# Kernel tuning notes

Hardware: AMD Instinct MI355X
Metric: run time of the kernel (lower is better)

The kernel has to match this reference:

```python
import jax, jax.numpy as jnp
import numpy as np

B, D_IN, H = 8192, 4096, 128
E, N, C = 3, 256, 32          # experts, codebook_size, codebook_dim
D1, D2 = 512, 256             # down_units
U1, U2 = 256, 512             # up_units
CW = 0.25                     # commitment_weight


def setup_inputs() -> dict:
    key = jax.random.key(0)
    ks = jax.random.split(key, 16)
    s = 0.02
    f32 = jnp.float32
    inp = {
        'x':   jax.random.normal(ks[0], (B, D_IN), f32),
        # llm_down MLP: 4096 -> 512 -> 256 -> 128 (ReLU on hiddens, linear out)
        'Wd1': jax.random.normal(ks[1], (D_IN, D1), f32) * s, 'bd1': jnp.zeros((D1,), f32),
        'Wd2': jax.random.normal(ks[2], (D1, D2), f32) * s,  'bd2': jnp.zeros((D2,), f32),
        'Wd3': jax.random.normal(ks[3], (D2, H), f32) * s,   'bd3': jnp.zeros((H,), f32),
        # per-expert VQ: project_in 128->32, codebook [256,32], project_out 32->128
        'Win':  jax.random.normal(ks[4], (E, H, C), f32) * s, 'bin_': jnp.zeros((E, C), f32),
        'codebook': jax.random.normal(ks[5], (E, N, C), f32),
        'Wout': jax.random.normal(ks[6], (E, C, H), f32) * s, 'bout': jnp.zeros((E, H), f32),
        # llm_up MLP: 128 -> 256 -> 512 -> 4096
        'Wu1': jax.random.normal(ks[7], (H, U1), f32) * s,   'bu1': jnp.zeros((U1,), f32),
        'Wu2': jax.random.normal(ks[8], (U1, U2), f32) * s,  'bu2': jnp.zeros((U2,), f32),
        'Wu3': jax.random.normal(ks[9], (U2, D_IN), f32) * s, 'bu3': jnp.zeros((D_IN,), f32),
    }
    return inp


def _decorrelation_loss(qemb):
    # qemb: [B, E, H]
    b, e, h = qemb.shape
    cen = qemb - qemb.mean(axis=0, keepdims=True)
    cen = cen.transpose(1, 0, 2).reshape(e, -1)          # [E, B*H]
    cov = (cen @ cen.T) / (b * h - 1)                    # [E, E]
    std = jnp.sqrt(jnp.diag(cov))
    std = jnp.where(std > 1e-8, std, 1.0)
    corr = cov / jnp.outer(std, std)
    c2 = corr ** 2
    return c2.sum() - jnp.diag(c2).sum()


def _vq_experts(latent, Win, bin_, codebook, Wout, bout):
    # latent: [B,H]; all experts share the same (unmasked) latent.
    xe = jnp.einsum('bh,ehc->ebc', latent, Win) + bin_[:, None, :]      # [E,B,C]
    d2 = ((xe ** 2).sum(-1)[..., None]
          - 2.0 * jnp.einsum('ebc,enc->ebn', xe, codebook)
          + (codebook ** 2).sum(-1)[:, None, :])                        # [E,B,N]
    idx = jnp.argmin(d2, axis=-1)                                       # [E,B]
    q = jax.vmap(lambda c, i: c[i])(codebook, idx)                      # [E,B,C] gather
    commit = CW * jnp.mean((jax.lax.stop_gradient(q) - xe) ** 2, axis=(1, 2)).sum()
    quant = xe + jax.lax.stop_gradient(q - xe)                          # straight-through
    qe = jnp.einsum('ebc,ech->ebh', quant, Wout) + bout[:, None, :]     # [E,B,H]
    return qe, idx, commit


def reference(x, Wd1, bd1, Wd2, bd2, Wd3, bd3, Win, bin_, codebook, Wout, bout,
              Wu1, bu1, Wu2, bu2, Wu3, bu3):
    h = jax.nn.relu(x @ Wd1 + bd1)
    h = jax.nn.relu(h @ Wd2 + bd2)
    latent = h @ Wd3 + bd3                                              # [B,128]
    qe, idx, total_commit = _vq_experts(latent, Win, bin_, codebook, Wout, bout)
    qemb = qe.transpose(1, 0, 2)                                        # [B,E,H]
    decorr = _decorrelation_loss(qemb)
    rl = qemb.mean(axis=1)                                              # [B,H]
    u = jax.nn.relu(rl @ Wu1 + bu1)
    u = jax.nn.relu(u @ Wu2 + bu2)
    recon = jnp.clip(u @ Wu3 + bu3, -1.0, 1.0)                          # [B,4096]
    return (recon, idx.T, total_commit, decorr)
```

## Files before the change

### kernel.cpp

```cpp
#include <hip/hip_runtime.h>
#include <hip/hip_bf16.h>

using bf16 = __hip_bfloat16;

typedef __bf16 bf16x8 __attribute__((ext_vector_type(8)));
typedef float  f32x4  __attribute__((ext_vector_type(4)));
typedef unsigned int u32x4 __attribute__((ext_vector_type(4)));
typedef unsigned long long u64;
typedef unsigned short u16;
typedef unsigned int u32;

__device__ __forceinline__ float b2f(bf16 v) { return __bfloat162float(v); }
__device__ __forceinline__ bf16  f2b(float v) { return __float2bfloat16(v); }
__device__ __forceinline__ u16   bits(bf16 v) { return __builtin_bit_cast(u16, v); }

static constexpr size_t SZ_WD1S = 512ull  * 8192  * 2;
static constexpr size_t SZ_WD2S = 256ull  * 1536  * 2;
static constexpr size_t SZ_WFUS = 128ull  * 768   * 2;
static constexpr size_t SZ_WU1T = 256ull  * 128   * 2;
static constexpr size_t SZ_WU2T = 512ull  * 256   * 2;
static constexpr size_t SZ_WU3T = 4096ull * 512   * 2;
static constexpr size_t SZ_H1S  = 8192ull * 1536  * 2;
static constexpr size_t SZ_H2S  = 8192ull * 768   * 2;
static constexpr size_t SZ_XE   = 8192ull * 128   * 4;
static constexpr size_t SZ_QEMB = 3ull * 8192 * 128 * 4;
static constexpr size_t SZ_RL   = 8192ull * 128   * 2;
static constexpr size_t SZ_U1   = 8192ull * 256   * 2;
static constexpr size_t SZ_U2   = 8192ull * 512   * 2;
static constexpr size_t SZ_CNRM = 768ull * 4;
static constexpr size_t SZ_BFUS = 128ull * 4;
static constexpr size_t SZ_PART = 4ull * 8192 * 512 * 4;

static constexpr size_t OFF_WD1S = 0;
static constexpr size_t OFF_WD2S = OFF_WD1S + SZ_WD1S;
static constexpr size_t OFF_WFUS = OFF_WD2S + SZ_WD2S;
static constexpr size_t OFF_WU1T = OFF_WFUS + SZ_WFUS;
static constexpr size_t OFF_WU2T = OFF_WU1T + SZ_WU1T;
static constexpr size_t OFF_WU3T = OFF_WU2T + SZ_WU2T;
static constexpr size_t OFF_H1S  = OFF_WU3T + SZ_WU3T;
static constexpr size_t OFF_H2S  = OFF_H1S  + SZ_H1S;
static constexpr size_t OFF_XE   = OFF_H2S  + SZ_H2S;
static constexpr size_t OFF_QEMB = OFF_XE   + SZ_XE;
static constexpr size_t OFF_RL   = OFF_QEMB + SZ_QEMB;
static constexpr size_t OFF_U1   = OFF_RL   + SZ_RL;
static constexpr size_t OFF_U2   = OFF_U1   + SZ_U1;
static constexpr size_t OFF_CNRM = OFF_U2   + SZ_U2;
static constexpr size_t OFF_BFUS = OFF_CNRM + ((SZ_CNRM + 255) & ~size_t(255));
static constexpr size_t OFF_STAT = OFF_BFUS + ((SZ_BFUS + 255) & ~size_t(255));
static constexpr size_t OFF_PART = OFF_STAT + 2048;

__global__ void wtrans_bf16(const float* __restrict__ in, bf16* __restrict__ out,
                            int K, int N)
{
    __shared__ float tile[32][33];
    const int tx = threadIdx.x, ty = threadIdx.y;
    const int n0 = blockIdx.x * 32, k0 = blockIdx.y * 32;
    #pragma unroll
    for (int i = 0; i < 32; i += 8)
        tile[ty + i][tx] = in[(size_t)(k0 + ty + i) * N + n0 + tx];
    __syncthreads();
    #pragma unroll
    for (int i = 0; i < 32; i += 8)
        out[(size_t)(n0 + ty + i) * K + k0 + tx] = f2b(tile[tx][ty + i]);
}

__global__ void wtrans_split3(const float* __restrict__ in, bf16* __restrict__ out,
                              int K, int N)
{
    __shared__ float tile[32][33];
    const int tx = threadIdx.x, ty = threadIdx.y;
    const int n0 = blockIdx.x * 32, k0 = blockIdx.y * 32;
    #pragma unroll
    for (int i = 0; i < 32; i += 8)
        tile[ty + i][tx] = in[(size_t)(k0 + ty + i) * N + n0 + tx];
    __syncthreads();
    #pragma unroll
    for (int i = 0; i < 32; i += 8) {
        const float v = tile[tx][ty + i];
        const bf16 hi = f2b(v);
        const bf16 lo = f2b(v - b2f(hi));
        bf16* o = out + (size_t)(n0 + ty + i) * 3 * K + 3 * (k0 + tx);
        o[0] = hi; o[1] = lo; o[2] = hi;
    }
}

__global__ void wtrans_hilo(const float* __restrict__ in, bf16* __restrict__ out,
                            int K, int N)
{
    __shared__ float tile[32][33];
    const int tx = threadIdx.x, ty = threadIdx.y;
    const int n0 = blockIdx.x * 32, k0 = blockIdx.y * 32;
    #pragma unroll
    for (int i = 0; i < 32; i += 8)
        tile[ty + i][tx] = in[(size_t)(k0 + ty + i) * N + n0 + tx];
    __syncthreads();
    const int kg = k0 >> 5;
    #pragma unroll
    for (int i = 0; i < 32; i += 8) {
        const float v = tile[tx][ty + i];
        const bf16 hi = f2b(v);
        const bf16 lo = f2b(v - b2f(hi));
        bf16* o = out + (size_t)(n0 + ty + i) * 8192 + kg * 64 + tx;
        o[0] = hi; o[32] = lo;
    }
}

__global__ void cnorm_kernel(const float* __restrict__ cb, float* __restrict__ cnorm)
{
    const int i = blockIdx.x * blockDim.x + threadIdx.x;
    if (i < 768) {
        float s = 0.f;
        for (int k = 0; k < 32; ++k) { const float v = cb[i * 32 + k]; s += v * v; }
        cnorm[i] = s;
    }
}

__global__ __launch_bounds__(256)
void wfuse_kernel(const float* __restrict__ Wd3, const float* __restrict__ bd3,
                  const float* __restrict__ Win, const float* __restrict__ bin_,
                  bf16* __restrict__ BtS, float* __restrict__ bfuse)
{
    const int n = blockIdx.x;
    const int t = threadIdx.x;
    if (n >= 96) {
        bf16* o = BtS + (size_t)n * 768 + 3 * t;
        o[0] = f2b(0.f); o[1] = f2b(0.f); o[2] = f2b(0.f);
        if (t == 0) bfuse[n] = 0.f;
        return;
    }
    const int e = n >> 5, c = n & 31;
    float s = 0.f;
    for (int h = 0; h < 128; ++h)
        s += Wd3[t * 128 + h] * Win[(size_t)(e * 128 + h) * 32 + c];
    const bf16 hi = f2b(s);
    const bf16 lo = f2b(s - b2f(hi));
    bf16* o = BtS + (size_t)n * 768 + 3 * t;
    o[0] = hi; o[1] = lo; o[2] = hi;
    if (t == 0) {
        float b = bin_[e * 32 + c];
        for (int h = 0; h < 128; ++h)
            b += bd3[h] * Win[(size_t)(e * 128 + h) * 32 + c];
        bfuse[n] = b;
    }
}

__global__ __launch_bounds__(256, 4)
void gemm1_x3(const float* __restrict__ A, const bf16* __restrict__ Bhl,
              float* __restrict__ part)
{
    __shared__ bf16 As[128 * 64];
    __shared__ bf16 Bs[128 * 64];
    const int t = threadIdx.x, lane = t & 63, w = t >> 6;
    const int bid = blockIdx.x + blockIdx.y * 4 + blockIdx.z * 256;
    const int xcd = bid & 7, j = bid >> 3;
    const int panel = xcd + 8 * (j >> 6);
    const int n0 = (panel & 3) * 128;
    const int kz = panel >> 2;
    const int m0 = (j & 63) * 128;
    const int wr = w >> 1, wc = w & 1, l15 = lane & 15, quad = lane >> 4;
    const int offh = ((quad ^ (l15 & 7)) << 3);
    const int offl = offh ^ 32;

    f32x4 acc[4][4];
    #pragma unroll
    for (int i = 0; i < 4; ++i)
        #pragma unroll
        for (int jj = 0; jj < 4; ++jj)
            #pragma unroll
            for (int r = 0; r < 4; ++r) acc[i][jj][r] = 0.f;

    const int arow = t >> 1, ahalf = t & 1, arx = arow & 7;
    bf16* const aw0 = As + arow * 64 + (((ahalf * 2 + 0) ^ arx) << 3);
    bf16* const aw1 = As + arow * 64 + (((ahalf * 2 + 1) ^ arx) << 3);
    bf16* const aw2 = As + arow * 64 + (((4 + ahalf * 2 + 0) ^ arx) << 3);
    bf16* const aw3 = As + arow * 64 + (((4 + ahalf * 2 + 1) ^ arx) << 3);

    int brow[4], bco[4];
    #pragma unroll
    for (int i = 0; i < 4; ++i) {
        const int p = i * 256 + t;
        brow[i] = p >> 3;
        bco[i] = ((p & 7) ^ (brow[i] & 7)) * 8;
    }

    const int s0 = kz * 32, s1 = s0 + 32;
    for (int ks = s0; ks < s1; ++ks) {
        const float* ap = A + (size_t)(m0 + arow) * 4096 + ks * 32 + ahalf * 16;
        float f[16];
        *(float4*)(f + 0)  = *(const float4*)(ap + 0);
        *(float4*)(f + 4)  = *(const float4*)(ap + 4);
        *(float4*)(f + 8)  = *(const float4*)(ap + 8);
        *(float4*)(f + 12) = *(const float4*)(ap + 12);
        #pragma unroll
        for (int i = 0; i < 4; ++i) {
            const bf16* gb = Bhl + (size_t)(n0 + brow[i]) * 8192 + ks * 64 + bco[i];
            __builtin_amdgcn_global_load_lds(
                (const __attribute__((address_space(1))) void*)gb,
                (__attribute__((address_space(3))) void*)(Bs + (size_t)(i * 256 + t) * 8), 16, 0, 0);
        }
        {
            u32x4 hv, lv;
            #pragma unroll
            for (int jj = 0; jj < 4; ++jj) {
                const bf16 h0 = f2b(f[2 * jj]), h1 = f2b(f[2 * jj + 1]);
                const u32 l0 = bits(f2b(f[2 * jj] - b2f(h0)));
                const u32 l1 = bits(f2b(f[2 * jj + 1] - b2f(h1)));
                hv[jj] = (u32)bits(h0) | ((u32)bits(h1) << 16);
                lv[jj] = l0 | (l1 << 16);
            }
            *(u32x4*)aw0 = hv; *(u32x4*)aw2 = lv;
            #pragma unroll
            for (int jj = 0; jj < 4; ++jj) {
                const bf16 h0 = f2b(f[8 + 2 * jj]), h1 = f2b(f[8 + 2 * jj + 1]);
                const u32 l0 = bits(f2b(f[8 + 2 * jj] - b2f(h0)));
                const u32 l1 = bits(f2b(f[8 + 2 * jj + 1] - b2f(h1)));
                hv[jj] = (u32)bits(h0) | ((u32)bits(h1) << 16);
                lv[jj] = l0 | (l1 << 16);
            }
            *(u32x4*)aw1 = hv; *(u32x4*)aw3 = lv;
        }
        __syncthreads();
        {
            bf16x8 ah[4], al[4];
            #pragma unroll
            for (int mi = 0; mi < 4; ++mi) {
                const bf16* ar = As + (wr * 64 + mi * 16 + l15) * 64;
                ah[mi] = *(const bf16x8*)(ar + offh);
                al[mi] = *(const bf16x8*)(ar + offl);
            }
            #pragma unroll
            for (int ni = 0; ni < 4; ++ni) {
                const bf16* br = Bs + (wc * 64 + ni * 16 + l15) * 64;
                const bf16x8 bh = *(const bf16x8*)(br + offh);
                const bf16x8 bl = *(const bf16x8*)(br + offl);
                #pragma unroll
                for (int mi = 0; mi < 4; ++mi) {
                    acc[mi][ni] = __builtin_amdgcn_mfma_f32_16x16x32_bf16(ah[mi], bh, acc[mi][ni], 0, 0, 0);
                    acc[mi][ni] = __builtin_amdgcn_mfma_f32_16x16x32_bf16(al[mi], bh, acc[mi][ni], 0, 0, 0);
                    acc[mi][ni] = __builtin_amdgcn_mfma_f32_16x16x32_bf16(ah[mi], bl, acc[mi][ni], 0, 0, 0);
                }
            }
        }
        __syncthreads();
    }

    float* op = part + (size_t)kz * (8192ull * 512);
    #pragma unroll
    for (int mi = 0; mi < 4; ++mi)
        #pragma unroll
        for (int ni = 0; ni < 4; ++ni) {
            const int col = n0 + wc * 64 + ni * 16 + l15;
            #pragma unroll
            for (int r = 0; r < 4; ++r) {
                const int row = m0 + wr * 64 + mi * 16 + quad * 4 + r;
                op[(size_t)row * 512 + col] = acc[mi][ni][r];
            }
        }
}

__global__ __launch_bounds__(256)
void h1_epi(const float* __restrict__ part, const float* __restrict__ bias,
            bf16* __restrict__ out)
{
    const int idx = blockIdx.x * 256 + threadIdx.x;
    const int r = idx >> 7, c4 = idx & 127;
    const size_t base = (size_t)r * 512 + c4 * 4;
    const float4 p0 = *(const float4*)(part + 0ull * 8192 * 512 + base);
    const float4 p1 = *(const float4*)(part + 1ull * 8192 * 512 + base);
    const float4 p2 = *(const float4*)(part + 2ull * 8192 * 512 + base);
    const float4 p3 = *(const float4*)(part + 3ull * 8192 * 512 + base);
    const float4 bv = *(const float4*)(bias + c4 * 4);
    float v[4];
    v[0] = p0.x + p1.x + p2.x + p3.x + bv.x;
    v[1] = p0.y + p1.y + p2.y + p3.y + bv.y;
    v[2] = p0.z + p1.z + p2.z + p3.z + bv.z;
    v[3] = p0.w + p1.w + p2.w + p3.w + bv.w;
    u64 h[4], l[4];
    #pragma unroll
    for (int j = 0; j < 4; ++j) {
        const float vv = v[j] > 0.f ? v[j] : 0.f;
        const bf16 hi = f2b(vv);
        h[j] = bits(hi);
        l[j] = bits(f2b(vv - b2f(hi)));
    }
    const u64 w0 = h[0] | (h[0] << 16) | (l[0] << 32) | (h[1] << 48);
    const u64 w1 = h[1] | (l[1] << 16) | (h[2] << 32) | (h[2] << 48);
    const u64 w2 = l[2] | (h[3] << 16) | (h[3] << 32) | (l[3] << 48);
    u64* dst = (u64*)(out + (size_t)r * 1536 + 12 * c4);
    dst[0] = w0; dst[1] = w1; dst[2] = w2;
}

template <int EPI, int RELU>
__global__ __launch_bounds__(256)
void gemm_bt(const bf16* __restrict__ A, const bf16* __restrict__ Bt,
             const float* __restrict__ bias, void* __restrict__ outp,
             int M, int N, int K)
{
    __shared__ bf16 As[128 * 64];
    __shared__ bf16 Bs[128 * 64];
    const int t = threadIdx.x, lane = t & 63, w = t >> 6;
    const int n0 = blockIdx.x * 128;
    const int m0 = blockIdx.y * 128;
    const int wr = w >> 1, wc = w & 1, l15 = lane & 15, quad = lane >> 4;
    const int l7 = l15 & 7;

    f32x4 acc[4][4];
    #pragma unroll
    for (int i = 0; i < 4; ++i)
        #pragma unroll
        for (int j = 0; j < 4; ++j)
            #pragma unroll
            for (int r = 0; r < 4; ++r) acc[i][j][r] = 0.f;

    int lrow[4], lcol[4];
    #pragma unroll
    for (int i = 0; i < 4; ++i) {
        const int c = i * 256 + t;
        lrow[i] = c >> 3;
        lcol[i] = ((c & 7) ^ (lrow[i] & 7)) * 8;
    }

    for (int k0 = 0; k0 < K; k0 += 64) {
        #pragma unroll
        for (int i = 0; i < 4; ++i) {
            const int c = i * 256 + t;
            const bf16* ga = A  + (size_t)(m0 + lrow[i]) * K + k0 + lcol[i];
            const bf16* gb = Bt + (size_t)(n0 + lrow[i]) * K + k0 + lcol[i];
            __builtin_amdgcn_global_load_lds(
                (const __attribute__((address_space(1))) void*)ga,
                (__attribute__((address_space(3))) void*)(As + (size_t)c * 8), 16, 0, 0);
            __builtin_amdgcn_global_load_lds(
                (const __attribute__((address_space(1))) void*)gb,
                (__attribute__((address_space(3))) void*)(Bs + (size_t)c * 8), 16, 0, 0);
        }
        __syncthreads();
        #pragma unroll
        for (int kk = 0; kk < 2; ++kk) {
            const int sw = (((kk << 2) | quad) ^ l7) << 3;
            bf16x8 af[4], bfr[4];
            #pragma unroll
            for (int mi = 0; mi < 4; ++mi)
                af[mi] = *(const bf16x8*)(As + (wr * 64 + mi * 16 + l15) * 64 + sw);
            #pragma unroll
            for (int ni = 0; ni < 4; ++ni)
                bfr[ni] = *(const bf16x8*)(Bs + (wc * 64 + ni * 16 + l15) * 64 + sw);
            #pragma unroll
            for (int mi = 0; mi < 4; ++mi)
                #pragma unroll
                for (int ni = 0; ni < 4; ++ni)
                    acc[mi][ni] = __builtin_amdgcn_mfma_f32_16x16x32_bf16(
                        af[mi], bfr[ni], acc[mi][ni], 0, 0, 0);
        }
        __syncthreads();
    }

    #pragma unroll
    for (int mi = 0; mi < 4; ++mi)
        #pragma unroll
        for (int ni = 0; ni < 4; ++ni) {
            const int col = n0 + wc * 64 + ni * 16 + l15;
            const float bv = bias[col];
            #pragma unroll
            for (int r = 0; r < 4; ++r) {
                const int row = m0 + wr * 64 + mi * 16 + quad * 4 + r;
                float v = acc[mi][ni][r] + bv;
                if (RELU) v = v > 0.f ? v : 0.f;
                if (EPI == 0) {
                    ((float*)outp)[(size_t)row * N + col] = v;
                } else if (EPI == 1) {
                    const bf16 hi = f2b(v);
                    const bf16 lo = f2b(v - b2f(hi));
                    bf16* o = (bf16*)outp + (size_t)row * 3 * N + 3 * col;
                    o[0] = hi; o[1] = hi; o[2] = lo;
                } else if (EPI == 2) {
                    ((bf16*)outp)[(size_t)row * N + col] = f2b(v);
                } else {
                    v = fminf(fmaxf(v, -1.f), 1.f);
                    ((float*)outp)[(size_t)row * N + col] = v;
                }
            }
        }
}

__global__ __launch_bounds__(256)
void vq2_kernel(const float* __restrict__ xe_buf, const float* __restrict__ cb,
                const float* __restrict__ cnorm, const float* __restrict__ Wout,
                const float* __restrict__ bout, float* __restrict__ qemb,
                float* __restrict__ idx_out, float* __restrict__ commit_acc)
{
    __shared__ float cb_s[256 * 36];
    __shared__ float wo_s[32 * 128];
    __shared__ float cn_s[256];
    __shared__ float bo_s[128];
    __shared__ float xe_s[4 * 32];
    __shared__ float q_s[4 * 32];
    __shared__ int   idx_s[4];
    __shared__ u64   wred[4][4];
    __shared__ float cred[256];

    const int e  = blockIdx.x >> 8;
    const int rb = blockIdx.x & 255;
    const int t = threadIdx.x, lane = t & 63, w = t >> 6;

    for (int j = t; j < 256 * 32; j += 256) {
        const int code = j >> 5, c = j & 31;
        cb_s[code * 36 + c] = cb[(size_t)e * 8192 + j];
    }
    for (int j = t; j < 4096; j += 256) wo_s[j] = Wout[(size_t)e * 4096 + j];
    cn_s[t] = cnorm[e * 256 + t];
    if (t < 128) bo_s[t] = bout[e * 128 + t];
    float commit_loc = 0.f;
    __syncthreads();

    for (int it = 0; it < 8; ++it) {
        const int r0 = rb * 32 + it * 4;
        if (t < 128) {
            const int r4 = t >> 5, c = t & 31;
            xe_s[r4 * 32 + c] = xe_buf[(size_t)(r0 + r4) * 128 + e * 32 + c];
        }
        __syncthreads();

        u64 key[4];
        {
            const float4* cp = (const float4*)(cb_s + t * 36);
            const float cn = cn_s[t];
            #pragma unroll
            for (int r4 = 0; r4 < 4; ++r4) {
                float dot = 0.f;
                #pragma unroll
                for (int c4 = 0; c4 < 8; ++c4) {
                    const float4 cv = cp[c4];
                    const float4 xv = *(const float4*)(xe_s + r4 * 32 + c4 * 4);
                    dot += xv.x * cv.x + xv.y * cv.y + xv.z * cv.z + xv.w * cv.w;
                }
                const float d = cn - 2.f * dot;
                u32 ub = __builtin_bit_cast(u32, d);
                ub = (ub & 0x80000000u) ? ~ub : (ub | 0x80000000u);
                key[r4] = ((u64)ub << 32) | (u32)t;
            }
        }
        #pragma unroll
        for (int off = 32; off; off >>= 1) {
            #pragma unroll
            for (int r4 = 0; r4 < 4; ++r4) {
                const u64 o = __shfl_down(key[r4], off, 64);
                if (o < key[r4]) key[r4] = o;
            }
        }
        if (lane == 0) {
            #pragma unroll
            for (int r4 = 0; r4 < 4; ++r4) wred[r4][w] = key[r4];
        }
        __syncthreads();
        if (t < 4) {
            u64 k = wred[t][0];
            #pragma unroll
            for (int ww = 1; ww < 4; ++ww) if (wred[t][ww] < k) k = wred[t][ww];
            const int code = (int)(k & 0xFFFFFFFFu);
            idx_s[t] = code;
            idx_out[(size_t)(r0 + t) * 3 + e] = (float)code;
        }
        __syncthreads();
        if (t < 128) {
            const int r4 = t >> 5, c = t & 31;
            const float q = cb_s[idx_s[r4] * 36 + c];
            q_s[r4 * 32 + c] = q;
            const float dd = q - xe_s[r4 * 32 + c];
            commit_loc += dd * dd;
        }
        __syncthreads();
        #pragma unroll
        for (int p = 0; p < 2; ++p) {
            const int j = p * 256 + t;
            const int r4 = j >> 7, h = j & 127;
            float s = bo_s[h];
            #pragma unroll
            for (int c = 0; c < 32; ++c) s += q_s[r4 * 32 + c] * wo_s[c * 128 + h];
            qemb[((size_t)e * 8192 + r0 + r4) * 128 + h] = s;
        }
        __syncthreads();
    }

    cred[t] = commit_loc;
    __syncthreads();
    for (int o = 128; o; o >>= 1) { if (t < o) cred[t] += cred[t + o]; __syncthreads(); }
    if (t == 0) atomicAdd(commit_acc, cred[0]);
}

__global__ __launch_bounds__(256)
void rlmean_kernel(const float* __restrict__ qemb, bf16* __restrict__ rl,
                   float* __restrict__ meanAcc)
{
    const int t = threadIdx.x, h = t & 127, half = t >> 7;
    const int r0 = blockIdx.x * 64;
    float a0 = 0.f, a1 = 0.f, a2 = 0.f;
    for (int r = r0 + half; r < r0 + 64; r += 2) {
        const float v0 = qemb[((size_t)0 * 8192 + r) * 128 + h];
        const float v1 = qemb[((size_t)1 * 8192 + r) * 128 + h];
        const float v2 = qemb[((size_t)2 * 8192 + r) * 128 + h];
        a0 += v0; a1 += v1; a2 += v2;
        rl[(size_t)r * 128 + h] = f2b((v0 + v1 + v2) * (1.f / 3.f));
    }
    __shared__ float red[3][256];
    red[0][t] = a0; red[1][t] = a1; red[2][t] = a2;
    __syncthreads();
    if (t < 128) {
        atomicAdd(&meanAcc[0 * 128 + h], red[0][t] + red[0][t + 128]);
        atomicAdd(&meanAcc[1 * 128 + h], red[1][t] + red[1][t + 128]);
        atomicAdd(&meanAcc[2 * 128 + h], red[2][t] + red[2][t + 128]);
    }
}

__global__ __launch_bounds__(256)
void gram_kernel(const float* __restrict__ qemb, const float* __restrict__ meanAcc,
                 double* __restrict__ gram)
{
    const int t = threadIdx.x;
    const int h = t & 127, half = t >> 7;
    const int b0 = blockIdx.x * 32;
    const float m0 = meanAcc[0 * 128 + h] * (1.f / 8192.f);
    const float m1 = meanAcc[1 * 128 + h] * (1.f / 8192.f);
    const float m2 = meanAcc[2 * 128 + h] * (1.f / 8192.f);
    float g[6] = {0, 0, 0, 0, 0, 0};
    for (int b = b0 + half; b < b0 + 32; b += 2) {
        const float v0 = qemb[((size_t)0 * 8192 + b) * 128 + h] - m0;
        const float v1 = qemb[((size_t)1 * 8192 + b) * 128 + h] - m1;
        const float v2 = qemb[((size_t)2 * 8192 + b) * 128 + h] - m2;
        g[0] += v0 * v0; g[1] += v0 * v1; g[2] += v0 * v2;
        g[3] += v1 * v1; g[4] += v1 * v2; g[5] += v2 * v2;
    }
    __shared__ float red[256];
    for (int i = 0; i < 6; ++i) {
        red[t] = g[i];
        __syncthreads();
        for (int o = 128; o; o >>= 1) { if (t < o) red[t] += red[t + o]; __syncthreads(); }
        if (t == 0) atomicAdd(&gram[i], (double)red[0]);
        __syncthreads();
    }
}

__global__ void final_kernel(const float* __restrict__ commit_acc,
                             const double* __restrict__ gram,
                             float* __restrict__ out2)
{
    if (threadIdx.x != 0 || blockIdx.x != 0) return;
    const double denom = 8192.0 * 128.0 - 1.0;
    const double c00 = gram[0] / denom, c01 = gram[1] / denom, c02 = gram[2] / denom;
    const double c11 = gram[3] / denom, c12 = gram[4] / denom, c22 = gram[5] / denom;
    double s0 = sqrt(c00), s1 = sqrt(c11), s2 = sqrt(c22);
    if (!(s0 > 1e-8)) s0 = 1.0;
    if (!(s1 > 1e-8)) s1 = 1.0;
    if (!(s2 > 1e-8)) s2 = 1.0;
    const double r01 = c01 / (s0 * s1), r02 = c02 / (s0 * s2), r12 = c12 / (s1 * s2);
    const double decorr = 2.0 * (r01 * r01 + r02 * r02 + r12 * r12);
    out2[0] = (float)((double)commit_acc[0] * (0.25 / (8192.0 * 32.0)));
    out2[1] = (float)decorr;
}

extern "C" void kernel_launch(void* const* d_in, const int* in_sizes, int n_in,
                              void* d_out, int out_size, void* d_ws, size_t ws_size,
                              hipStream_t stream)
{
    const float* x    = (const float*)d_in[0];
    const float* Wd1  = (const float*)d_in[1];
    const float* bd1  = (const float*)d_in[2];
    const float* Wd2  = (const float*)d_in[3];
    const float* bd2  = (const float*)d_in[4];
    const float* Wd3  = (const float*)d_in[5];
    const float* bd3  = (const float*)d_in[6];
    const float* Win  = (const float*)d_in[7];
    const float* bin_ = (const float*)d_in[8];
    const float* cb   = (const float*)d_in[9];
    const float* Wout = (const float*)d_in[10];
    const float* bout = (const float*)d_in[11];
    const float* Wu1  = (const float*)d_in[12];
    const float* bu1  = (const float*)d_in[13];
    const float* Wu2  = (const float*)d_in[14];
    const float* bu2  = (const float*)d_in[15];
    const float* Wu3  = (const float*)d_in[16];
    const float* bu3  = (const float*)d_in[17];

    char* ws = (char*)d_ws;
    bf16*  Wd1s   = (bf16*)(ws + OFF_WD1S);
    bf16*  Wd2s   = (bf16*)(ws + OFF_WD2S);
    bf16*  WfuseS = (bf16*)(ws + OFF_WFUS);
    bf16*  Wu1T   = (bf16*)(ws + OFF_WU1T);
    bf16*  Wu2T   = (bf16*)(ws + OFF_WU2T);
    bf16*  Wu3T   = (bf16*)(ws + OFF_WU3T);
    bf16*  h1s    = (bf16*)(ws + OFF_H1S);
    bf16*  h2s    = (bf16*)(ws + OFF_H2S);
    float* xe     = (float*)(ws + OFF_XE);
    float* qemb   = (float*)(ws + OFF_QEMB);
    bf16*  rl     = (bf16*)(ws + OFF_RL);
    bf16*  u1     = (bf16*)(ws + OFF_U1);
    bf16*  u2     = (bf16*)(ws + OFF_U2);
    float* cnorm  = (float*)(ws + OFF_CNRM);
    float* bfuse  = (float*)(ws + OFF_BFUS);
    float* commit = (float*)(ws + OFF_STAT);
    double* gram  = (double*)(ws + OFF_STAT + 8);
    float* meanA  = (float*)(ws + OFF_STAT + 64);
    float* part   = (float*)(ws + OFF_PART);

    float* out_f   = (float*)d_out;
    float* idx_out = out_f + (size_t)8192 * 4096;
    float* scal    = idx_out + (size_t)8192 * 3;

    hipMemsetAsync(ws + OFF_STAT, 0, 2048, stream);

    const dim3 tb(32, 8);
    wtrans_hilo<<<dim3(16, 128), tb, 0, stream>>>(Wd1, Wd1s, 4096, 512);
    wtrans_split3<<<dim3(8, 16),   tb, 0, stream>>>(Wd2, Wd2s, 512, 256);
    wtrans_bf16<<<dim3(8, 4),      tb, 0, stream>>>(Wu1, Wu1T, 128, 256);
    wtrans_bf16<<<dim3(16, 8),     tb, 0, stream>>>(Wu2, Wu2T, 256, 512);
    wtrans_bf16<<<dim3(128, 16),   tb, 0, stream>>>(Wu3, Wu3T, 512, 4096);
    cnorm_kernel<<<3, 256, 0, stream>>>(cb, cnorm);
    wfuse_kernel<<<128, 256, 0, stream>>>(Wd3, bd3, Win, bin_, WfuseS, bfuse);

    gemm1_x3<<<dim3(4, 64, 4), 256, 0, stream>>>(x, Wd1s, part);
    h1_epi<<<4096, 256, 0, stream>>>(part, bd1, h1s);
    gemm_bt<1, 1><<<dim3(2, 64), 256, 0, stream>>>(h1s, Wd2s, bd2, h2s, 8192, 256, 1536);
    gemm_bt<0, 0><<<dim3(1, 64), 256, 0, stream>>>(h2s, WfuseS, bfuse, xe, 8192, 128, 768);

    vq2_kernel<<<768, 256, 0, stream>>>(xe, cb, cnorm, Wout, bout, qemb, idx_out, commit);
    rlmean_kernel<<<128, 256, 0, stream>>>(qemb, rl, meanA);
    gram_kernel<<<256, 256, 0, stream>>>(qemb, meanA, gram);
    final_kernel<<<1, 64, 0, stream>>>(commit, gram, scal);

    gemm_bt<2, 1><<<dim3(2, 64),  256, 0, stream>>>(rl, Wu1T, bu1, u1,    8192, 256,  128);
    gemm_bt<2, 1><<<dim3(4, 64),  256, 0, stream>>>(u1, Wu2T, bu2, u2,    8192, 512,  256);
    gemm_bt<3, 0><<<dim3(32, 64), 256, 0, stream>>>(u2, Wu3T, bu3, out_f, 8192, 4096, 512);

    (void)in_sizes; (void)n_in; (void)out_size; (void)ws_size;
}
```

Before: 586.8 us.

## Prefetch next A tile into registers and remap block-to-XCD assignment in gemm1

```diff
diff --git a/kernel.cpp b/kernel.cpp
--- a/kernel.cpp
+++ b/kernel.cpp
@@ -152,11 +152,11 @@
     __shared__ bf16 Bs[128 * 64];
     const int t = threadIdx.x, lane = t & 63, w = t >> 6;
     const int bid = blockIdx.x + blockIdx.y * 4 + blockIdx.z * 256;
-    const int xcd = bid & 7, j = bid >> 3;
-    const int panel = xcd + 8 * (j >> 6);
-    const int n0 = (panel & 3) * 128;
-    const int kz = panel >> 2;
-    const int m0 = (j & 63) * 128;
+    const int xcd = bid & 7;
+    const int r   = bid >> 3;
+    const int kz  = xcd >> 1;
+    const int m0  = ((xcd & 1) * 32 + (r >> 2)) * 128;
+    const int n0  = (r & 3) * 128;
     const int wr = w >> 1, wc = w & 1, l15 = lane & 15, quad = lane >> 4;
     const int offh = ((quad ^ (l15 & 7)) << 3);
     const int offl = offh ^ 32;
@@ -167,7 +167,7 @@
         #pragma unroll
         for (int jj = 0; jj < 4; ++jj)
             #pragma unroll
-            for (int r = 0; r < 4; ++r) acc[i][jj][r] = 0.f;
+            for (int rr = 0; rr < 4; ++rr) acc[i][jj][rr] = 0.f;
 
     const int arow = t >> 1, ahalf = t & 1, arx = arow & 7;
     bf16* const aw0 = As + arow * 64 + (((ahalf * 2 + 0) ^ arx) << 3);
@@ -184,19 +184,33 @@
     }
 
     const int s0 = kz * 32, s1 = s0 + 32;
-    for (int ks = s0; ks < s1; ++ks) {
-        const float* ap = A + (size_t)(m0 + arow) * 4096 + ks * 32 + ahalf * 16;
-        float f[16];
+    const float* const apbase = A + (size_t)(m0 + arow) * 4096 + ahalf * 16;
+
+    float f[16];
+    {
+        const float* ap = apbase + s0 * 32;
         *(float4*)(f + 0)  = *(const float4*)(ap + 0);
         *(float4*)(f + 4)  = *(const float4*)(ap + 4);
         *(float4*)(f + 8)  = *(const float4*)(ap + 8);
         *(float4*)(f + 12) = *(const float4*)(ap + 12);
+    }
+
+    for (int ks = s0; ks < s1; ++ks) {
+        const bool haveNext = (ks + 1 < s1);
         #pragma unroll
         for (int i = 0; i < 4; ++i) {
             const bf16* gb = Bhl + (size_t)(n0 + brow[i]) * 8192 + ks * 64 + bco[i];
             __builtin_amdgcn_global_load_lds(
                 (const __attribute__((address_space(1))) void*)gb,
                 (__attribute__((address_space(3))) void*)(Bs + (size_t)(i * 256 + t) * 8), 16, 0, 0);
+        }
+        float g[16];
+        if (haveNext) {
+            const float* ap = apbase + (ks + 1) * 32;
+            *(float4*)(g + 0)  = *(const float4*)(ap + 0);
+            *(float4*)(g + 4)  = *(const float4*)(ap + 4);
+            *(float4*)(g + 8)  = *(const float4*)(ap + 8);
+            *(float4*)(g + 12) = *(const float4*)(ap + 12);
         }
         {
             u32x4 hv, lv;
@@ -242,6 +256,10 @@
             }
         }
         __syncthreads();
+        if (haveNext) {
+            #pragma unroll
+            for (int k = 0; k < 16; ++k) f[k] = g[k];
+        }
     }
 
     float* op = part + (size_t)kz * (8192ull * 512);
@@ -251,9 +269,9 @@
         for (int ni = 0; ni < 4; ++ni) {
             const int col = n0 + wc * 64 + ni * 16 + l15;
             #pragma unroll
-            for (int r = 0; r < 4; ++r) {
-                const int row = m0 + wr * 64 + mi * 16 + quad * 4 + r;
-                op[(size_t)row * 512 + col] = acc[mi][ni][r];
+            for (int rr = 0; rr < 4; ++rr) {
+                const int row = m0 + wr * 64 + mi * 16 + quad * 4 + rr;
+                op[(size_t)row * 512 + col] = acc[mi][ni][rr];
             }
         }
 }
```

New measurement: 1.090 ms. 85.7% more time.
